# Optimization experiments

Measured on AMD Instinct MI355X. Metric: run time of the kernel, lower is better.

Reference implementation:

```python
import jax, jax.numpy as jnp
import numpy as np

N_NODES = 200000
N_EDGES = 6400000
IN_CH, HID, OUT_CH = 14, 16, 2


def gcn_conv(x, W, b, src, dst, n_nodes):
    """GCNConv with self-loops and symmetric normalization (PyG defaults).

    out[i] = sum_{j->i} d[i]^-1/2 d[j]^-1/2 (xW)[j] + d[i]^-1 (xW)[i] + b,
    where d = degree(A + I) computed on the target index.
    """
    h = x @ W  # [N, F_out]
    ones = jnp.ones((src.shape[0],), dtype=x.dtype)
    deg = jax.ops.segment_sum(ones, dst, num_segments=n_nodes) + 1.0  # +1 self-loop
    dinv = jax.lax.rsqrt(deg)  # [N]
    norm = dinv[src] * dinv[dst]  # [E]
    msg = h[src] * norm[:, None]  # [E, F_out] -- dominant memory traffic
    agg = jax.ops.segment_sum(msg, dst, num_segments=n_nodes)
    self_loop = h * (dinv * dinv)[:, None]
    return agg + self_loop + b


def setup_inputs() -> dict:
    key = jax.random.key(0)
    k1, k2, k3, k4, k5 = jax.random.split(key, 5)
    x = jax.random.normal(k1, (N_NODES, IN_CH), dtype=jnp.float32)
    edge_index = jax.random.randint(k2, (2, N_EDGES), 0, N_NODES, dtype=jnp.int64)
    edge_attr = jax.random.normal(k3, (N_EDGES, 1), dtype=jnp.float32)  # unused by GCNConv
    s = 1.0 / np.sqrt(IN_CH)
    W1 = jax.random.uniform(k4, (IN_CH, HID), jnp.float32, -s, s)
    b1 = jnp.zeros((HID,), jnp.float32)
    s2 = 1.0 / np.sqrt(HID)
    W2 = jax.random.uniform(k5, (HID, OUT_CH), jnp.float32, -s2, s2)
    b2 = jnp.zeros((OUT_CH,), jnp.float32)
    return {"x": x, "edge_index": edge_index, "edge_attr": edge_attr,
            "W1": W1, "b1": b1, "W2": W2, "b2": b2}


def reference(x, edge_index, edge_attr, W1, b1, W2, b2):
    src, dst = edge_index[0], edge_index[1]
    n = x.shape[0]
    h = jax.nn.relu(gcn_conv(x, W1, b1, src, dst, n))
    # F.dropout(training=self.training) is identity in eval mode
    out = gcn_conv(h, W2, b2, src, dst, n)
    return out
```

## Files before the change

kernel.cpp:

```cpp
#include <hip/hip_runtime.h>
#include <hip/hip_fp16.h>


constexpr int NN = 200000;
constexpr int NE = 6400000;
constexpr int IC = 14;
constexpr int HC = 16;
constexpr int OC = 2;

constexpr int NBK = 392;
constexpr int NSUB = 8;
constexpr int SCAP = 2816;
constexpr int NSEG = NSUB * NBK;
constexpr int CCAP = NSUB * SCAP;
constexpr int SPT = (SCAP + 1023) / 1024;
constexpr int TILE = 5120;
constexpr int BTH = 512;
constexpr int IPT = TILE / BTH;
constexpr int IPT2 = IPT / 2;
constexpr int NTILE = NE / TILE;
constexpr int OVFCAP = 65536;
constexpr int NM = NN / 32;
constexpr int GSTR = 16;

typedef unsigned long long ull;
typedef float f4v __attribute__((ext_vector_type(4)));

__device__ __forceinline__ int phase_of(unsigned src) {
    return src >= 100000u ? (src >= 150000u ? 3 : 2) : (src >= 50000u ? 1 : 0);
}

__device__ __forceinline__ int xcc_id() {
    int x;
    asm volatile("s_getreg_b32 %0, hwreg(HW_REG_XCC_ID)" : "=s"(x));
    return x & 7;
}

__global__ void k_init(int* __restrict__ gcur, const void* __restrict__ ei,
                       int* __restrict__ flag) {
    int i = blockIdx.x * blockDim.x + threadIdx.x;
    if (i < NSEG) gcur[i * GSTR] = i * SCAP;
    else if (i <= NSEG + 4) gcur[i * GSTR] = 0;
    if (i == 500) {
        const ull* p = (const ull*)ei;
        ull acc = 0ULL;
        for (int k = 0; k < 64; ++k) acc |= (p[k] >> 32);
        *flag = (acc == 0ULL) ? 1 : 0;
    }
}

__global__ __launch_bounds__(BTH, 8) void k_binA(const void* __restrict__ ei,
                                                 const int* __restrict__ flag,
                                                 int* __restrict__ gcur,
                                                 unsigned* __restrict__ binned,
                                                 ull* __restrict__ ovf) {
    __shared__ int hist[NBK];
    __shared__ int lofs[NBK];
    __shared__ int gofs[NBK];
    __shared__ int wsum[BTH / 64];
    __shared__ unsigned stage[TILE];

    int t = threadIdx.x;
    int fl = *flag;
    int tile0 = blockIdx.x * TILE;
    int segbase = xcc_id() * NBK;

    if (t < NBK) hist[t] = 0;
    __syncthreads();

    unsigned pk[IPT];
    unsigned ra[IPT];
#pragma unroll
    for (int k = 0; k < IPT2; ++k) {
        int e = tile0 + k * (2 * BTH) + 2 * t;
        int d0, d1, s0, s1;
        if (fl) {
            ulonglong2 dd = *(const ulonglong2*)((const long long*)ei + NE + e);
            ulonglong2 ss = *(const ulonglong2*)((const long long*)ei + e);
            d0 = (int)dd.x;
            d1 = (int)dd.y;
            s0 = (int)ss.x;
            s1 = (int)ss.y;
        } else {
            uint2 dd = *(const uint2*)((const int*)ei + NE + e);
            uint2 ss = *(const uint2*)((const int*)ei + e);
            d0 = (int)dd.x;
            d1 = (int)dd.y;
            s0 = (int)ss.x;
            s1 = (int)ss.y;
        }
        int b0 = d0 >> 9, b1 = d1 >> 9;
        int r0 = atomicAdd(&hist[b0], 1);
        int r1 = atomicAdd(&hist[b1], 1);
        pk[2 * k] = ((unsigned)(d0 & 511) << 18) | (unsigned)s0;
        pk[2 * k + 1] = ((unsigned)(d1 & 511) << 18) | (unsigned)s1;
        ra[2 * k] = ((unsigned)r0 << 9) | (unsigned)b0;
        ra[2 * k + 1] = ((unsigned)r1 << 9) | (unsigned)b1;
    }
    __syncthreads();

    int h0 = 0, h1 = 0, p = 0;
    if (t < NBK / 2) {
        h0 = hist[2 * t];
        h1 = hist[2 * t + 1];
        p = h0 + h1;
    }
    int lane = t & 63;
    int w = t >> 6;
    int incl = p;
#pragma unroll
    for (int off = 1; off < 64; off <<= 1) {
        int v = __shfl_up(incl, off, 64);
        if (lane >= off) incl += v;
    }
    if (lane == 63) wsum[w] = incl;
    __syncthreads();
    int wbase = 0;
#pragma unroll
    for (int ww = 0; ww < BTH / 64; ++ww) wbase += (ww < w) ? wsum[ww] : 0;
    int ex = wbase + incl - p;
    if (t < NBK / 2) {
        lofs[2 * t] = ex;
        lofs[2 * t + 1] = ex + h0;
    }
    if (t < NBK) gofs[t] = atomicAdd(&gcur[(segbase + t) * GSTR], hist[t]);
    __syncthreads();

#pragma unroll
    for (int k = 0; k < IPT; ++k) {
        int b = (int)(ra[k] & 511u);
        int r = (int)(ra[k] >> 9);
        stage[lofs[b] + r] = pk[k];
    }
    __syncthreads();

    for (int i = t; i < TILE; i += BTH) {
        int b = (i * 313) >> 12;
        if (b > NBK - 1) b = NBK - 1;
        while (b < NBK - 1 && lofs[b + 1] <= i) ++b;
        while (lofs[b] > i) --b;
        unsigned pack = stage[i];
        int seg = segbase + b;
        int dest = gofs[b] + (i - lofs[b]);
        if (dest < (seg + 1) * SCAP) {
            binned[dest] = pack;
        } else {
            int op = atomicAdd(&gcur[NSEG * GSTR], 1);
            if (op < OVFCAP) {
                int d = (b << 9) | (int)(pack >> 18);
                int s = (int)(pack & 0x3FFFF);
                ovf[op] = ((ull)d << 32) | (unsigned)s;
            }
        }
    }
}

__global__ __launch_bounds__(1024, 4) void k_sort(const int* __restrict__ gcur,
                                                  const unsigned* __restrict__ binned,
                                                  const ull* __restrict__ ovf,
                                                  unsigned* __restrict__ csr,
                                                  float* __restrict__ dinv,
                                                  int* __restrict__ rsg,
                                                  unsigned* __restrict__ spl) {
    __shared__ int cnt[2048];
    __shared__ int excl[2048];
    __shared__ int wsum[16];
    __shared__ int nseg[NSUB];
    __shared__ unsigned stage[CCAP];
    int b = blockIdx.x;
    int t = threadIdx.x;
    cnt[t] = 0;
    cnt[t + 1024] = 0;
    if (t < NSUB) {
        int seg = t * NBK + b;
        nseg[t] = min(gcur[seg * GSTR] - seg * SCAP, SCAP);
    }
    __syncthreads();
    int nov = min(gcur[NSEG * GSTR], OVFCAP);

    unsigned srcv[NSUB * SPT];
    unsigned rkv[NSUB * SPT];
#pragma unroll
    for (int s = 0; s < NSUB; ++s) {
        int n = nseg[s];
        int sb = (s * NBK + b) * SCAP;
#pragma unroll
        for (int k = 0; k < SPT; ++k) {
            int i = k * 1024 + t;
            rkv[s * SPT + k] = 0xFFFFFFFFu;
            if (i < n) {
                unsigned pack = binned[sb + i];
                unsigned src = pack & 0x3FFFFu;
                int key = ((int)(pack >> 18) << 2) | phase_of(src);
                int r = atomicAdd(&cnt[key], 1);
                srcv[s * SPT + k] = src;
                rkv[s * SPT + k] = ((unsigned)r << 11) | (unsigned)key;
            }
        }
    }
    __syncthreads();

    int h0 = cnt[2 * t];
    int h1 = cnt[2 * t + 1];
    int p = h0 + h1;
    int lane = t & 63;
    int w = t >> 6;
    int incl = p;
#pragma unroll
    for (int off = 1; off < 64; off <<= 1) {
        int v = __shfl_up(incl, off, 64);
        if (lane >= off) incl += v;
    }
    if (lane == 63) wsum[w] = incl;
    __syncthreads();
    int wbase = 0;
#pragma unroll
    for (int ww = 0; ww < 16; ++ww) wbase += (ww < w) ? wsum[ww] : 0;
    int ex = wbase + incl - p;
    excl[2 * t] = ex;
    excl[2 * t + 1] = ex + h0;
    __syncthreads();

#pragma unroll
    for (int c = 0; c < NSUB * SPT; ++c) {
        unsigned rk = rkv[c];
        if (rk != 0xFFFFFFFFu) {
            int key = (int)(rk & 0x7FFu);
            int r = (int)(rk >> 11);
            stage[excl[key] + r] = srcv[c];
        }
    }

    if (t < 512) {
        int g = (b << 9) + t;
        if (g < NN) {
            int c0 = cnt[4 * t];
            int c1 = cnt[4 * t + 1];
            int c2 = cnt[4 * t + 2];
            int c3 = cnt[4 * t + 3];
            int extra = 0;
            for (int k = 0; k < nov; ++k) extra += ((int)(ovf[k] >> 32) == g);
            dinv[g] = rsqrtf((float)(c0 + c1 + c2 + c3 + extra) + 1.0f);
            rsg[g] = b * CCAP + excl[4 * t];
            spl[g] = (unsigned)c0 | ((unsigned)c1 << 8) |
                     ((unsigned)c2 << 16) | ((unsigned)c3 << 24);
        }
    }
    __syncthreads();

    int total = excl[2047] + cnt[2047];
    int tot4 = (total + 3) >> 2;
    const uint4* st4 = (const uint4*)stage;
    uint4* csr4 = (uint4*)(csr + (size_t)b * CCAP);
#pragma unroll
    for (int k = 0; k < (CCAP / 4 + 1023) / 1024; ++k) {
        int i4 = k * 1024 + t;
        if (i4 < tot4) csr4[i4] = st4[i4];
    }
}

__global__ void k_prep(const float* __restrict__ x, const float* __restrict__ dinv,
                       __half* __restrict__ xph) {
    int i = blockIdx.x * blockDim.x + threadIdx.x;
    if (i >= NN * 16) return;
    int node = i >> 4;
    int c = i & 15;
    float v = (c < IC) ? dinv[node] * x[node * IC + c] : 0.0f;
    xph[i] = __float2half(v);
}

__global__ __launch_bounds__(256) void k_agg1(const int* __restrict__ rsg,
                                              const unsigned* __restrict__ spl,
                                              const unsigned* __restrict__ csr,
                                              const __half* __restrict__ xph,
                                              float* __restrict__ partial) {
    int t = threadIdx.x;
    int q2 = blockIdx.x & 1;
    int blk = blockIdx.x >> 1;
    int g = t >> 3;
    int qq = t & 3;
    int eh = (t >> 2) & 1;
    int i = blk * 32 + g;
    unsigned sp = spl[i];
    int c0 = (int)(sp & 255u);
    int c1 = (int)((sp >> 8) & 255u);
    int beg = rsg[i] + (q2 ? c0 : 0);
    int end = beg + (q2 ? c1 : c0);

    float ax = 0.0f, ay = 0.0f, az = 0.0f, aw = 0.0f;
    int j = beg + eh;
    for (; j + 2 < end; j += 4) {
        int s0 = csr[j];
        int s1 = csr[j + 2];
        uint2 u0 = *(const uint2*)(xph + (size_t)s0 * 16 + 4 * qq);
        uint2 u1 = *(const uint2*)(xph + (size_t)s1 * 16 + 4 * qq);
        float2 f0 = __half22float2(*(__half2*)&u0.x);
        float2 f1 = __half22float2(*(__half2*)&u0.y);
        float2 f2 = __half22float2(*(__half2*)&u1.x);
        float2 f3 = __half22float2(*(__half2*)&u1.y);
        ax += f0.x + f2.x;
        ay += f0.y + f2.y;
        az += f1.x + f3.x;
        aw += f1.y + f3.y;
    }
    if (j < end) {
        int s0 = csr[j];
        uint2 u0 = *(const uint2*)(xph + (size_t)s0 * 16 + 4 * qq);
        float2 f0 = __half22float2(*(__half2*)&u0.x);
        float2 f1 = __half22float2(*(__half2*)&u0.y);
        ax += f0.x;
        ay += f0.y;
        az += f1.x;
        aw += f1.y;
    }
    ax += __shfl_xor(ax, 4);
    ay += __shfl_xor(ay, 4);
    az += __shfl_xor(az, 4);
    aw += __shfl_xor(aw, 4);
    if (eh == 0) {
        f4v r = {ax, ay, az, aw};
        __builtin_nontemporal_store(
            r, (f4v*)(partial + ((size_t)q2 * NN + i) * 16 + 4 * qq));
    }
}

__global__ __launch_bounds__(256) void k_agg1m(const int* __restrict__ rsg,
                                               const unsigned* __restrict__ spl,
                                               const unsigned* __restrict__ csr,
                                               const __half* __restrict__ xph,
                                               const float* __restrict__ partial,
                                               const int* __restrict__ gcur,
                                               const ull* __restrict__ ovf,
                                               const float* __restrict__ dinv,
                                               const float* __restrict__ W1,
                                               const float* __restrict__ b1,
                                               const float* __restrict__ W2,
                                               const float* __restrict__ b2,
                                               float2* __restrict__ h2bp,
                                               float2* __restrict__ selfout) {
    __shared__ float sW1[IC * HC];
    __shared__ float sb1[HC];
    __shared__ float sW2[HC * OC];
    __shared__ float sb2[OC];
    __shared__ float sAgg[32][17];
    int t = threadIdx.x;
    if (t < IC * HC) sW1[t] = W1[t];
    if (t < HC) sb1[t] = b1[t];
    if (t < HC * OC) sW2[t] = W2[t];
    if (t < OC) sb2[t] = b2[t];

    int g = t >> 3;
    int qq = t & 3;
    int eh = (t >> 2) & 1;
    int i = blockIdx.x * 32 + g;
    unsigned sp = spl[i];
    int c0 = (int)(sp & 255u);
    int c1 = (int)((sp >> 8) & 255u);
    int c2 = (int)((sp >> 16) & 255u);
    int c3 = (int)(sp >> 24);
    int beg = rsg[i] + c0 + c1;
    int end = beg + c2 + c3;

    float ax = 0.0f, ay = 0.0f, az = 0.0f, aw = 0.0f;
    int j = beg + eh;
    for (; j + 2 < end; j += 4) {
        int s0 = csr[j];
        int s1 = csr[j + 2];
        uint2 u0 = *(const uint2*)(xph + (size_t)s0 * 16 + 4 * qq);
        uint2 u1 = *(const uint2*)(xph + (size_t)s1 * 16 + 4 * qq);
        float2 f0 = __half22float2(*(__half2*)&u0.x);
        float2 f1 = __half22float2(*(__half2*)&u0.y);
        float2 f2 = __half22float2(*(__half2*)&u1.x);
        float2 f3 = __half22float2(*(__half2*)&u1.y);
        ax += f0.x + f2.x;
        ay += f0.y + f2.y;
        az += f1.x + f3.x;
        aw += f1.y + f3.y;
    }
    if (j < end) {
        int s0 = csr[j];
        uint2 u0 = *(const uint2*)(xph + (size_t)s0 * 16 + 4 * qq);
        float2 f0 = __half22float2(*(__half2*)&u0.x);
        float2 f1 = __half22float2(*(__half2*)&u0.y);
        ax += f0.x;
        ay += f0.y;
        az += f1.x;
        aw += f1.y;
    }

    if (eh == 0) {
        f4v a0 = __builtin_nontemporal_load(
            (const f4v*)(partial + (size_t)i * 16 + 4 * qq));
        uint2 us = *(const uint2*)(xph + (size_t)i * 16 + 4 * qq);
        float2 sx = __half22float2(*(__half2*)&us.x);
        float2 sy = __half22float2(*(__half2*)&us.y);
        ax += a0.x + sx.x;
        ay += a0.y + sx.y;
        az += a0.z + sy.x;
        aw += a0.w + sy.y;
    } else {
        f4v a1 = __builtin_nontemporal_load(
            (const f4v*)(partial + ((size_t)NN + i) * 16 + 4 * qq));
        ax += a1.x;
        ay += a1.y;
        az += a1.z;
        aw += a1.w;
    }
    ax += __shfl_xor(ax, 4);
    ay += __shfl_xor(ay, 4);
    az += __shfl_xor(az, 4);
    aw += __shfl_xor(aw, 4);

    float dv = dinv[i];
    if (eh == 0) {
        int nov = min(gcur[NSEG * GSTR], OVFCAP);
        for (int k = 0; k < nov; ++k) {
            ull e = ovf[k];
            if ((int)(e >> 32) == i) {
                int s = (int)(e & 0xFFFFFFFFu);
                int ch = 4 * qq;
                ax += __half2float(xph[(size_t)s * 16 + ch]);
                ay += __half2float(xph[(size_t)s * 16 + ch + 1]);
                az += __half2float(xph[(size_t)s * 16 + ch + 2]);
                aw += __half2float(xph[(size_t)s * 16 + ch + 3]);
            }
        }
        sAgg[g][4 * qq + 0] = dv * ax;
        sAgg[g][4 * qq + 1] = dv * ay;
        sAgg[g][4 * qq + 2] = dv * az;
        sAgg[g][4 * qq + 3] = dv * aw;
    }
    __syncthreads();

    int l8 = t & 7;
    float o0 = 0.0f, o1 = 0.0f;
#pragma unroll
    for (int f2 = 0; f2 < 2; ++f2) {
        int f = 2 * l8 + f2;
        float a = sb1[f];
#pragma unroll
        for (int c = 0; c < IC; ++c) a = fmaf(sAgg[g][c], sW1[c * HC + f], a);
        a = fmaxf(a, 0.0f);
        o0 = fmaf(a, sW2[f * OC + 0], o0);
        o1 = fmaf(a, sW2[f * OC + 1], o1);
    }
    o0 += __shfl_xor(o0, 1);
    o1 += __shfl_xor(o1, 1);
    o0 += __shfl_xor(o0, 2);
    o1 += __shfl_xor(o1, 2);
    o0 += __shfl_xor(o0, 4);
    o1 += __shfl_xor(o1, 4);
    if (l8 == 0) {
        h2bp[i] = make_float2(o0 * dv, o1 * dv);
        selfout[i] = make_float2(o0 * dv * dv + sb2[0], o1 * dv * dv + sb2[1]);
    }
}

__global__ __launch_bounds__(256) void k_agg2(const int* __restrict__ rsg,
                                              const unsigned* __restrict__ spl,
                                              const unsigned* __restrict__ csr,
                                              const int* __restrict__ gcur,
                                              const ull* __restrict__ ovf,
                                              const float* __restrict__ dinv,
                                              const float2* __restrict__ h2bp,
                                              const float2* __restrict__ selfout,
                                              float2* __restrict__ out) {
    int tt = blockIdx.x * 256 + threadIdx.x;
    int i = tt >> 3;
    int h = tt & 7;
    if (i >= NN) return;
    unsigned sp = spl[i];
    int tot = (int)(sp & 255u) + (int)((sp >> 8) & 255u) +
              (int)((sp >> 16) & 255u) + (int)(sp >> 24);
    int beg = rsg[i];
    int end = beg + tot;
    float ax = 0.0f, ay = 0.0f;
    int j = beg + h;
    for (; j + 8 < end; j += 16) {
        int s0 = csr[j];
        int s1 = csr[j + 8];
        float2 h0 = h2bp[s0];
        float2 h1 = h2bp[s1];
        ax += h0.x + h1.x;
        ay += h0.y + h1.y;
    }
    if (j < end) {
        float2 h0 = h2bp[csr[j]];
        ax += h0.x;
        ay += h0.y;
    }
    ax += __shfl_xor(ax, 1);
    ay += __shfl_xor(ay, 1);
    ax += __shfl_xor(ax, 2);
    ay += __shfl_xor(ay, 2);
    ax += __shfl_xor(ax, 4);
    ay += __shfl_xor(ay, 4);
    if (h == 0) {
        int nov = min(gcur[NSEG * GSTR], OVFCAP);
        for (int k = 0; k < nov; ++k) {
            ull e = ovf[k];
            if ((int)(e >> 32) == i) {
                float2 hh = h2bp[(int)(e & 0xFFFFFFFFu)];
                ax += hh.x;
                ay += hh.y;
            }
        }
        float dv = dinv[i];
        float2 so = selfout[i];
        out[i] = make_float2(so.x + dv * ax, so.y + dv * ay);
    }
}

extern "C" void kernel_launch(void* const* d_in, const int* in_sizes, int n_in,
                              void* d_out, int out_size, void* d_ws, size_t ws_size,
                              hipStream_t stream) {
    const float* x = (const float*)d_in[0];
    const void* ei = d_in[1];
    const float* W1 = (const float*)d_in[3];
    const float* b1 = (const float*)d_in[4];
    const float* W2 = (const float*)d_in[5];
    const float* b2 = (const float*)d_in[6];
    float* out = (float*)d_out;

    ull* ovf = (ull*)d_ws;
    int* gcur = (int*)(ovf + OVFCAP);
    int* flag = gcur + (NSEG + 5) * GSTR;
    int* rsg = flag + 4;
    unsigned* spl = (unsigned*)(rsg + NN);
    float* dinv = (float*)(spl + NN);
    __half* xph = (__half*)(dinv + NN);
    float2* h2bp = (float2*)(xph + (size_t)NN * 16);
    float2* selfout = h2bp + NN;
    unsigned* binned = (unsigned*)(selfout + NN);
    float* partial = (float*)binned;
    unsigned* csr = binned + (size_t)NSEG * SCAP;

    k_init<<<(NSEG + 5 + 255) / 256, 256, 0, stream>>>(gcur, ei, flag);
    k_binA<<<NTILE, BTH, 0, stream>>>(ei, flag, gcur, binned, ovf);
    k_sort<<<NBK, 1024, 0, stream>>>(gcur, binned, ovf, csr, dinv, rsg, spl);
    k_prep<<<(NN * 16 + 255) / 256, 256, 0, stream>>>(x, dinv, xph);
    k_agg1<<<2 * NM, 256, 0, stream>>>(rsg, spl, csr, xph, partial);
    k_agg1m<<<NM, 256, 0, stream>>>(rsg, spl, csr, xph, partial, gcur, ovf, dinv,
                                    W1, b1, W2, b2, h2bp, selfout);
    k_agg2<<<(NN * 8 + 255) / 256, 256, 0, stream>>>(rsg, spl, csr, gcur, ovf, dinv,
                                                     h2bp, selfout, (float2*)out);
}
```

Measured before the change: 290.2 us.

## Software-pipeline CSR index loads in gather loops and batch edge loads in binning

The three gather kernels now prefetch the next iteration's CSR source indices before doing the current iteration's feature gathers. This is meant to hide the dependent index-then-feature load latency. The binning kernel issues all edge index loads up front before the shared-memory histogram atomics, and reads only the low 32-bit words for int64 input. It also lowers the launch-bounds occupancy hint from 8 to 6 to leave room for the extra registers. The risks are higher register pressure, lower occupancy, and an added branch on the odd second gather.

New measurement: 285.0 us. Within noise of the previous version (-1.8%).

```diff
diff --git a/kernel.cpp b/kernel.cpp
--- a/kernel.cpp
+++ b/kernel.cpp
@@ -49,7 +49,7 @@
     }
 }
 
-__global__ __launch_bounds__(BTH, 8) void k_binA(const void* __restrict__ ei,
+__global__ __launch_bounds__(BTH, 6) void k_binA(const void* __restrict__ ei,
                                                  const int* __restrict__ flag,
                                                  int* __restrict__ gcur,
                                                  unsigned* __restrict__ binned,
@@ -68,34 +68,39 @@
     if (t < NBK) hist[t] = 0;
     __syncthreads();
 
+    int dbuf[IPT], sbuf[IPT];
+    const int* pw = (const int*)ei;
+    if (fl) {
+#pragma unroll
+        for (int k = 0; k < IPT2; ++k) {
+            int e = tile0 + k * (2 * BTH) + 2 * t;
+            dbuf[2 * k] = pw[2 * (NE + e)];
+            dbuf[2 * k + 1] = pw[2 * (NE + e) + 2];
+            sbuf[2 * k] = pw[2 * e];
+            sbuf[2 * k + 1] = pw[2 * e + 2];
+        }
+    } else {
+#pragma unroll
+        for (int k = 0; k < IPT2; ++k) {
+            int e = tile0 + k * (2 * BTH) + 2 * t;
+            uint2 dd = *(const uint2*)(pw + NE + e);
+            uint2 ss = *(const uint2*)(pw + e);
+            dbuf[2 * k] = (int)dd.x;
+            dbuf[2 * k + 1] = (int)dd.y;
+            sbuf[2 * k] = (int)ss.x;
+            sbuf[2 * k + 1] = (int)ss.y;
+        }
+    }
+
     unsigned pk[IPT];
     unsigned ra[IPT];
 #pragma unroll
-    for (int k = 0; k < IPT2; ++k) {
-        int e = tile0 + k * (2 * BTH) + 2 * t;
-        int d0, d1, s0, s1;
-        if (fl) {
-            ulonglong2 dd = *(const ulonglong2*)((const long long*)ei + NE + e);
-            ulonglong2 ss = *(const ulonglong2*)((const long long*)ei + e);
-            d0 = (int)dd.x;
-            d1 = (int)dd.y;
-            s0 = (int)ss.x;
-            s1 = (int)ss.y;
-        } else {
-            uint2 dd = *(const uint2*)((const int*)ei + NE + e);
-            uint2 ss = *(const uint2*)((const int*)ei + e);
-            d0 = (int)dd.x;
-            d1 = (int)dd.y;
-            s0 = (int)ss.x;
-            s1 = (int)ss.y;
-        }
-        int b0 = d0 >> 9, b1 = d1 >> 9;
-        int r0 = atomicAdd(&hist[b0], 1);
-        int r1 = atomicAdd(&hist[b1], 1);
-        pk[2 * k] = ((unsigned)(d0 & 511) << 18) | (unsigned)s0;
-        pk[2 * k + 1] = ((unsigned)(d1 & 511) << 18) | (unsigned)s1;
-        ra[2 * k] = ((unsigned)r0 << 9) | (unsigned)b0;
-        ra[2 * k + 1] = ((unsigned)r1 << 9) | (unsigned)b1;
+    for (int k = 0; k < IPT; ++k) {
+        int d = dbuf[k];
+        int b = d >> 9;
+        int r = atomicAdd(&hist[b], 1);
+        pk[k] = ((unsigned)(d & 511) << 18) | (unsigned)sbuf[k];
+        ra[k] = ((unsigned)r << 9) | (unsigned)b;
     }
     __syncthreads();
 
@@ -289,22 +294,12 @@
 
     float ax = 0.0f, ay = 0.0f, az = 0.0f, aw = 0.0f;
     int j = beg + eh;
-    for (; j + 2 < end; j += 4) {
-        int s0 = csr[j];
-        int s1 = csr[j + 2];
-        uint2 u0 = *(const uint2*)(xph + (size_t)s0 * 16 + 4 * qq);
-        uint2 u1 = *(const uint2*)(xph + (size_t)s1 * 16 + 4 * qq);
-        float2 f0 = __half22float2(*(__half2*)&u0.x);
-        float2 f1 = __half22float2(*(__half2*)&u0.y);
-        float2 f2 = __half22float2(*(__half2*)&u1.x);
-        float2 f3 = __half22float2(*(__half2*)&u1.y);
-        ax += f0.x + f2.x;
-        ay += f0.y + f2.y;
-        az += f1.x + f3.x;
-        aw += f1.y + f3.y;
-    }
-    if (j < end) {
-        int s0 = csr[j];
+    int s0 = (j < end) ? (int)csr[j] : -1;
+    int s1 = (j + 2 < end) ? (int)csr[j + 2] : -1;
+    while (j < end) {
+        int jn = j + 4;
+        int n0 = (jn < end) ? (int)csr[jn] : -1;
+        int n1 = (jn + 2 < end) ? (int)csr[jn + 2] : -1;
         uint2 u0 = *(const uint2*)(xph + (size_t)s0 * 16 + 4 * qq);
         float2 f0 = __half22float2(*(__half2*)&u0.x);
         float2 f1 = __half22float2(*(__half2*)&u0.y);
@@ -312,6 +307,18 @@
         ay += f0.y;
         az += f1.x;
         aw += f1.y;
+        if (s1 >= 0) {
+            uint2 u1 = *(const uint2*)(xph + (size_t)s1 * 16 + 4 * qq);
+            float2 f2 = __half22float2(*(__half2*)&u1.x);
+            float2 f3 = __half22float2(*(__half2*)&u1.y);
+            ax += f2.x;
+            ay += f2.y;
+            az += f3.x;
+            aw += f3.y;
+        }
+        s0 = n0;
+        s1 = n1;
+        j = jn;
     }
     ax += __shfl_xor(ax, 4);
     ay += __shfl_xor(ay, 4);
@@ -363,22 +370,12 @@
 
     float ax = 0.0f, ay = 0.0f, az = 0.0f, aw = 0.0f;
     int j = beg + eh;
-    for (; j + 2 < end; j += 4) {
-        int s0 = csr[j];
-        int s1 = csr[j + 2];
-        uint2 u0 = *(const uint2*)(xph + (size_t)s0 * 16 + 4 * qq);
-        uint2 u1 = *(const uint2*)(xph + (size_t)s1 * 16 + 4 * qq);
-        float2 f0 = __half22float2(*(__half2*)&u0.x);
-        float2 f1 = __half22float2(*(__half2*)&u0.y);
-        float2 f2 = __half22float2(*(__half2*)&u1.x);
-        float2 f3 = __half22float2(*(__half2*)&u1.y);
-        ax += f0.x + f2.x;
-        ay += f0.y + f2.y;
-        az += f1.x + f3.x;
-        aw += f1.y + f3.y;
-    }
-    if (j < end) {
-        int s0 = csr[j];
+    int s0 = (j < end) ? (int)csr[j] : -1;
+    int s1 = (j + 2 < end) ? (int)csr[j + 2] : -1;
+    while (j < end) {
+        int jn = j + 4;
+        int n0 = (jn < end) ? (int)csr[jn] : -1;
+        int n1 = (jn + 2 < end) ? (int)csr[jn + 2] : -1;
         uint2 u0 = *(const uint2*)(xph + (size_t)s0 * 16 + 4 * qq);
         float2 f0 = __half22float2(*(__half2*)&u0.x);
         float2 f1 = __half22float2(*(__half2*)&u0.y);
@@ -386,6 +383,18 @@
         ay += f0.y;
         az += f1.x;
         aw += f1.y;
+        if (s1 >= 0) {
+            uint2 u1 = *(const uint2*)(xph + (size_t)s1 * 16 + 4 * qq);
+            float2 f2 = __half22float2(*(__half2*)&u1.x);
+            float2 f3 = __half22float2(*(__half2*)&u1.y);
+            ax += f2.x;
+            ay += f2.y;
+            az += f3.x;
+            aw += f3.y;
+        }
+        s0 = n0;
+        s1 = n1;
+        j = jn;
     }
 
     if (eh == 0) {
@@ -476,18 +485,23 @@
     int end = beg + tot;
     float ax = 0.0f, ay = 0.0f;
     int j = beg + h;
-    for (; j + 8 < end; j += 16) {
-        int s0 = csr[j];
-        int s1 = csr[j + 8];
+    int s0 = (j < end) ? (int)csr[j] : -1;
+    int s1 = (j + 8 < end) ? (int)csr[j + 8] : -1;
+    while (j < end) {
+        int jn = j + 16;
+        int n0 = (jn < end) ? (int)csr[jn] : -1;
+        int n1 = (jn + 8 < end) ? (int)csr[jn + 8] : -1;
         float2 h0 = h2bp[s0];
-        float2 h1 = h2bp[s1];
-        ax += h0.x + h1.x;
-        ay += h0.y + h1.y;
-    }
-    if (j < end) {
-        float2 h0 = h2bp[csr[j]];
         ax += h0.x;
         ay += h0.y;
+        if (s1 >= 0) {
+            float2 h1 = h2bp[s1];
+            ax += h1.x;
+            ay += h1.y;
+        }
+        s0 = n0;
+        s1 = n1;
+        j = jn;
     }
     ax += __shfl_xor(ax, 1);
     ay += __shfl_xor(ay, 1);
```
